# Kernel tuning notes

Measured on AMD Instinct MI355X. Metric: run time of the kernel, lower is better.

The kernel has to match this reference:

```python
import jax, jax.numpy as jnp
import numpy as np

K = 5          # reassembly kernel size
S = 2          # scale factor
ENC_PAD = 1    # encoder_kernel_size // 2


def _conv2d(x, w, pad):
    return jax.lax.conv_general_dilated(
        x, w, window_strides=(1, 1), padding=[(pad, pad), (pad, pad)],
        dimension_numbers=('NCHW', 'OIHW', 'NCHW'))


def setup_inputs() -> dict:
    key = jax.random.key(0)
    k1, k2, k3 = jax.random.split(key, 3)
    x = jax.random.normal(k1, (2, 256, 40, 40), dtype=jnp.float32)
    # channel compressor: xavier-uniform-ish 1x1 conv weight (64, 256, 1, 1)
    limit = np.sqrt(6.0 / (256 + 64)).astype(np.float32)
    w_comp = jax.random.uniform(k2, (64, 256, 1, 1), dtype=jnp.float32,
                                minval=-limit, maxval=limit)
    # content encoder: normal(0, 0.001), out = k^2*s^2 = 100 channels
    w_enc = 0.001 * jax.random.normal(k3, (100, 64, 3, 3), dtype=jnp.float32)
    return {"x": x, "w_comp": w_comp, "w_enc": w_enc}


def reference(x, w_comp, w_enc):
    b, c, h, w = x.shape
    k2 = K * K
    h_up, w_up = h * S, w * S

    # --- kernel prediction ---
    compressed = _conv2d(x, w_comp, 0)                # (b, 64, h, w)
    kern = _conv2d(compressed, w_enc, ENC_PAD)        # (b, k2*S^2, h, w)
    # pixel shuffle: (b, k2, S, S, h, w) -> (b, k2, h, S, w, S) -> (b, k2, h_up, w_up)
    kern = kern.reshape(b, k2, S, S, h, w).transpose(0, 1, 4, 2, 5, 3)
    kern = kern.reshape(b, k2, h_up * w_up)
    kern = jax.nn.softmax(kern, axis=1)               # softmax over k2

    # --- unfold (im2col, padding K//2) ---
    pad = K // 2
    xp = jnp.pad(x, ((0, 0), (0, 0), (pad, pad), (pad, pad)))
    # (b, c, k2, h, w): channel-major, kernel offsets inner (matches torch F.unfold)
    patches = jnp.stack([xp[:, :, i:i + h, j:j + w]
                         for i in range(K) for j in range(K)], axis=2)
    x_unfold = patches.reshape(b, c, k2, h * w)

    # --- reassembly (faithful to the torch 'efficient' path) ---
    # torch repeat_interleaves x_unfold S^2 times along the h*w axis and
    # multiplies with kernels flattened in (h_up*w_up) row-major order; that
    # pairing is exactly kern reshaped to (b, k2, h*w, S^2):
    kern4 = kern.reshape(b, k2, h * w, S * S)
    out = jnp.einsum('bckp,bkpd->bcpd', x_unfold, kern4)  # (b, c, h*w, S^2)
    return out.reshape(b, c, h_up, w_up)
```

## Files before the change

kernel.cpp:

```cpp
#include <hip/hip_runtime.h>

#define B   2
#define C   256
#define CM  64
#define CE  100
#define H   40
#define W   40
#define HW  1600
#define KK  25

__global__ __launch_bounds__(256) void k1_conv1x1(
    const float* __restrict__ x, const float* __restrict__ w,
    float* __restrict__ pc) {
  const int t = blockIdx.x, ich = blockIdx.y, b = blockIdx.z;
  __shared__ __align__(16) float xs[64 * 64];
  __shared__ __align__(16) float wsA[64 * 64];
  const int tid = threadIdx.x;

  const float4* x4 = (const float4*)(x + ((size_t)b * C + ich * 64) * HW + t * 64);
#pragma unroll
  for (int i = 0; i < 4; i++) {
    int idx = tid + i * 256;
    ((float4*)xs)[idx] = x4[(idx >> 4) * 400 + (idx & 15)];
  }
  const float4* w4 = (const float4*)w;
#pragma unroll
  for (int i = 0; i < 4; i++) {
    int idx = tid + i * 256;
    int icq = idx >> 6, oc = idx & 63;
    float4 f = w4[oc * 64 + ich * 16 + icq];
    wsA[(icq * 4 + 0) * 64 + oc] = f.x;
    wsA[(icq * 4 + 1) * 64 + oc] = f.y;
    wsA[(icq * 4 + 2) * 64 + oc] = f.z;
    wsA[(icq * 4 + 3) * 64 + oc] = f.w;
  }
  __syncthreads();

  const int ty = tid >> 4, tx = tid & 15;
  float acc[4][4];
#pragma unroll
  for (int i = 0; i < 4; i++)
#pragma unroll
    for (int j = 0; j < 4; j++) acc[i][j] = 0.f;

#pragma unroll 4
  for (int icl = 0; icl < 64; icl++) {
    float4 a = *(const float4*)&wsA[icl * 64 + ty * 4];
    float4 bb = *(const float4*)&xs[icl * 64 + tx * 4];
    float av[4] = {a.x, a.y, a.z, a.w};
    float bv[4] = {bb.x, bb.y, bb.z, bb.w};
#pragma unroll
    for (int i = 0; i < 4; i++)
#pragma unroll
      for (int j = 0; j < 4; j++) acc[i][j] += av[i] * bv[j];
  }

  float* o = pc + ((size_t)ich * B + b) * CM * HW + t * 64 + tx * 4;
#pragma unroll
  for (int j = 0; j < 4; j++)
    *(float4*)&o[(size_t)(ty * 4 + j) * HW] =
        make_float4(acc[j][0], acc[j][1], acc[j][2], acc[j][3]);
}

__global__ __launch_bounds__(256) void k2_conv3x3(
    const float* __restrict__ pc, const float* __restrict__ w,
    float* __restrict__ encP) {
  const int tile = blockIdx.x, ocq = blockIdx.y, icq = blockIdx.z;
  const int ty5 = tile / 5, tx5 = tile % 5;
  __shared__ __align__(16) float smem[3200 + 16 * 9 * 28];
  float* cs  = smem;
  float* wsb = smem + 3200;
  float* pacc = smem;
  const int tid = threadIdx.x;

  for (int i = tid; i < 3200; i += 256) {
    int bb = i / 1600, r = i - bb * 1600;
    int icl = r / 100, rr = r - icl * 100;
    int yy = rr / 10, xx = rr - yy * 10;
    int gy = ty5 * 8 + yy - 1, gx = tx5 * 8 + xx - 1;
    float v = 0.f;
    if (gy >= 0 && gy < H && gx >= 0 && gx < W) {
      int o = bb * 102400 + (icq * 16 + icl) * HW + gy * W + gx;
      v = pc[o] + pc[204800 + o] + pc[409600 + o] + pc[614400 + o];
    }
    cs[i] = v;
  }
  const float* wb = w + (size_t)(ocq * 25) * 576 + (size_t)(icq * 16) * 9;
  for (int i = tid; i < 3600; i += 256) {
    int ol = i / 144, r = i - ol * 144;
    wsb[r * 28 + ol] = wb[ol * 576 + r];
  }
  __syncthreads();

  const int wv = tid >> 6, lane = tid & 63, py = lane >> 3, px = lane & 7;
  float acc[50];
#pragma unroll
  for (int j = 0; j < 50; j++) acc[j] = 0.f;

#pragma unroll 1
  for (int t = 0; t < 4; t++) {
    const int icl = wv * 4 + t;
    const float* c0 = &cs[icl * 100 + py * 10 + px];
    const float* c1 = c0 + 1600;
    const float* wrow = &wsb[icl * 9 * 28];
#pragma unroll
    for (int dy = 0; dy < 3; dy++) {
#pragma unroll
      for (int dx = 0; dx < 3; dx++) {
        float x0 = c0[dy * 10 + dx];
        float x1 = c1[dy * 10 + dx];
        const float* wp = &wrow[(dy * 3 + dx) * 28];
        float4 w0 = *(const float4*)&wp[0],  w1 = *(const float4*)&wp[4];
        float4 w2 = *(const float4*)&wp[8],  w3 = *(const float4*)&wp[12];
        float4 w4v = *(const float4*)&wp[16], w5 = *(const float4*)&wp[20];
        float w6 = wp[24];
        acc[0]  += x0 * w0.x;  acc[1]  += x0 * w0.y;  acc[2]  += x0 * w0.z;  acc[3]  += x0 * w0.w;
        acc[4]  += x0 * w1.x;  acc[5]  += x0 * w1.y;  acc[6]  += x0 * w1.z;  acc[7]  += x0 * w1.w;
        acc[8]  += x0 * w2.x;  acc[9]  += x0 * w2.y;  acc[10] += x0 * w2.z;  acc[11] += x0 * w2.w;
        acc[12] += x0 * w3.x;  acc[13] += x0 * w3.y;  acc[14] += x0 * w3.z;  acc[15] += x0 * w3.w;
        acc[16] += x0 * w4v.x; acc[17] += x0 * w4v.y; acc[18] += x0 * w4v.z; acc[19] += x0 * w4v.w;
        acc[20] += x0 * w5.x;  acc[21] += x0 * w5.y;  acc[22] += x0 * w5.z;  acc[23] += x0 * w5.w;
        acc[24] += x0 * w6;
        acc[25] += x1 * w0.x;  acc[26] += x1 * w0.y;  acc[27] += x1 * w0.z;  acc[28] += x1 * w0.w;
        acc[29] += x1 * w1.x;  acc[30] += x1 * w1.y;  acc[31] += x1 * w1.z;  acc[32] += x1 * w1.w;
        acc[33] += x1 * w2.x;  acc[34] += x1 * w2.y;  acc[35] += x1 * w2.z;  acc[36] += x1 * w2.w;
        acc[37] += x1 * w3.x;  acc[38] += x1 * w3.y;  acc[39] += x1 * w3.z;  acc[40] += x1 * w3.w;
        acc[41] += x1 * w4v.x; acc[42] += x1 * w4v.y; acc[43] += x1 * w4v.z; acc[44] += x1 * w4v.w;
        acc[45] += x1 * w5.x;  acc[46] += x1 * w5.y;  acc[47] += x1 * w5.z;  acc[48] += x1 * w5.w;
        acc[49] += x1 * w6;
      }
    }
  }

  __syncthreads();
  if (wv == 1 || wv == 3) {
    const int slot = wv >> 1;
#pragma unroll
    for (int j = 0; j < 50; j++) pacc[slot * 3200 + j * 64 + lane] = acc[j];
  }
  __syncthreads();
  if (wv == 0 || wv == 2) {
    const int slot = wv >> 1;
#pragma unroll
    for (int j = 0; j < 50; j++) acc[j] += pacc[slot * 3200 + j * 64 + lane];
  }
  __syncthreads();
  if (wv == 2) {
#pragma unroll
    for (int j = 0; j < 50; j++) pacc[j * 64 + lane] = acc[j];
  }
  __syncthreads();
  if (wv == 0) {
    const int base_px = (ty5 * 8 + py) * W + tx5 * 8 + px;
#pragma unroll
    for (int bb = 0; bb < 2; bb++)
#pragma unroll
      for (int ol = 0; ol < 25; ol++)
        encP[(((size_t)icq * 2 + bb) * CE + ocq * 25 + ol) * HW + base_px] =
            acc[bb * 25 + ol] + pacc[(bb * 25 + ol) * 64 + lane];
  }
}

__global__ __launch_bounds__(256) void k3_reassemble(
    const float* __restrict__ x, const float* __restrict__ encP,
    float* __restrict__ out) {
  const int i0 = blockIdx.x >> 1;
  const int jh = blockIdx.x & 1;
  const int cq = blockIdx.y;
  const int b = blockIdx.z;

  __shared__ __align__(16) float wlds[20 * KK * 4];
  __shared__ float xsm[64 * 121];

  const int tid = threadIdx.x;

  if (tid < 80) {
    const int e = jh * 80 + tid;
    const int j0 = e >> 2, d = e & 3;
    const int off = ((e >= 80) ? 2 : 0) + (e & 1);
    const int col = ((e >= 80) ? (j0 - 20) : j0) * 2 + (d >> 1);
    const float* ep = encP + (size_t)b * CE * HW + i0 * W + col;
    float v[KK];
    float m = -1e30f;
#pragma unroll
    for (int k = 0; k < KK; k++) {
      int o = (k * 4 + off) * HW;
      v[k] = ep[o] + ep[320000 + o] + ep[640000 + o] + ep[960000 + o];
      m = fmaxf(m, v[k]);
    }
    float s = 0.f;
#pragma unroll
    for (int k = 0; k < KK; k++) {
      v[k] = expf(v[k] - m);
      s += v[k];
    }
    const float inv = 1.f / s;
    const int j0l = j0 - jh * 20;
#pragma unroll
    for (int k = 0; k < KK; k++) wlds[(j0l * KK + k) * 4 + d] = v[k] * inv;
  }

  const float* xb = x + ((size_t)b * C + cq * 64) * HW;
  for (int i = tid; i < 64 * 120; i += 256) {
    int c = i / 120;
    int rr = i % 120;
    int r = rr / 24, t = rr % 24;
    int gy = i0 - 2 + r;
    int gx = jh * 20 + t - 2;
    float v = 0.f;
    if (gy >= 0 && gy < H && gx >= 0 && gx < W) v = xb[c * HW + gy * W + gx];
    xsm[c * 121 + r * 24 + t] = v;
  }
  __syncthreads();

  const int wv = tid >> 6;
  const int lane = tid & 63;
  float* ob = out + (((size_t)b * C + cq * 64 + lane) * 6400) + i0 * 160;
  const float* xrow = &xsm[lane * 121];
#pragma unroll 1
  for (int jj = 0; jj < 5; jj++) {
    const int j0l = wv * 5 + jj;
    const int j0 = jh * 20 + j0l;
    float a0 = 0.f, a1 = 0.f, a2 = 0.f, a3 = 0.f;
#pragma unroll
    for (int ki = 0; ki < 5; ki++) {
#pragma unroll
      for (int kj = 0; kj < 5; kj++) {
        float xv = xrow[ki * 24 + j0l + kj];
        float4 w4 = *(const float4*)&wlds[(j0l * KK + ki * 5 + kj) * 4];
        a0 += xv * w4.x;
        a1 += xv * w4.y;
        a2 += xv * w4.z;
        a3 += xv * w4.w;
      }
    }
    float4 o = make_float4(a0, a1, a2, a3);
    *(float4*)&ob[j0 * 4] = o;
  }
}

extern "C" void kernel_launch(void* const* d_in, const int* in_sizes, int n_in,
                              void* d_out, int out_size, void* d_ws, size_t ws_size,
                              hipStream_t stream) {
  const float* x      = (const float*)d_in[0];
  const float* w_comp = (const float*)d_in[1];
  const float* w_enc  = (const float*)d_in[2];
  float* out = (float*)d_out;

  float* pc   = (float*)d_ws;
  float* encP = (float*)((char*)d_ws + 3276800);

  k1_conv1x1<<<dim3(25, 4, B), 256, 0, stream>>>(x, w_comp, pc);
  k2_conv3x3<<<dim3(25, 4, 4), 256, 0, stream>>>(pc, w_enc, encP);
  k3_reassemble<<<dim3(80, 4, B), 256, 0, stream>>>(x, encP, out);
}
```

Before: 109.7 us.

## Pre-transpose encoder weights, retile conv3x3 and reassembly across all channels

Adds a small kernel that transposes the 3x3 encoder weights into a padded layout in workspace, so the conv3x3 kernel reads weights straight from global memory with wave-uniform addresses instead of staging them in LDS. The conv3x3 grid doubles with smaller 8x4 spatial tiles and 25 accumulators per thread, which lowers register pressure and raises occupancy. The reassembly kernel is restructured so each block covers all 256 channels for 4 output columns. Each thread computes 4 channels times 4 sub-pixels, which reuses the softmax weights across more channels and cuts redundant softmax work. The cost is an extra kernel launch, and the reassembly's strided per-channel loads of x may coalesce poorly.

```diff
diff --git a/kernel.cpp b/kernel.cpp
--- a/kernel.cpp
+++ b/kernel.cpp
@@ -9,6 +9,16 @@
 #define HW  1600
 #define KK  25
 
+__global__ __launch_bounds__(256) void k0_wt(const float* __restrict__ w,
+                                             float* __restrict__ wT) {
+  int idx = blockIdx.x * 256 + threadIdx.x;
+  if (idx < 57600) {
+    int row = idx / 576, col = idx - row * 576;
+    int ocq = row / 25, ol = row - ocq * 25;
+    wT[((size_t)(ocq * 576 + col)) * 32 + ol] = w[idx];
+  }
+}
+
 __global__ __launch_bounds__(256) void k1_conv1x1(
     const float* __restrict__ x, const float* __restrict__ w,
     float* __restrict__ pc) {
@@ -63,21 +73,20 @@
 }
 
 __global__ __launch_bounds__(256) void k2_conv3x3(
-    const float* __restrict__ pc, const float* __restrict__ w,
+    const float* __restrict__ pc, const float* __restrict__ wT,
     float* __restrict__ encP) {
-  const int tile = blockIdx.x, ocq = blockIdx.y, icq = blockIdx.z;
-  const int ty5 = tile / 5, tx5 = tile % 5;
-  __shared__ __align__(16) float smem[3200 + 16 * 9 * 28];
-  float* cs  = smem;
-  float* wsb = smem + 3200;
+  const int t = blockIdx.x, ocq = blockIdx.y, icq = blockIdx.z;
+  const int ty = t / 10, tx = t - ty * 10;
+  __shared__ __align__(16) float smem[3200];
+  float* cs   = smem;
   float* pacc = smem;
   const int tid = threadIdx.x;
 
-  for (int i = tid; i < 3200; i += 256) {
-    int bb = i / 1600, r = i - bb * 1600;
-    int icl = r / 100, rr = r - icl * 100;
-    int yy = rr / 10, xx = rr - yy * 10;
-    int gy = ty5 * 8 + yy - 1, gx = tx5 * 8 + xx - 1;
+  for (int i = tid; i < 1920; i += 256) {
+    int bb = i / 960, r = i - bb * 960;
+    int icl = r / 60, rr = r - icl * 60;
+    int yy = rr / 6, xx = rr - yy * 6;
+    int gy = ty * 8 + yy - 1, gx = tx * 4 + xx - 1;
     float v = 0.f;
     if (gy >= 0 && gy < H && gx >= 0 && gx < W) {
       int o = bb * 102400 + (icq * 16 + icl) * HW + gy * W + gx;
@@ -85,100 +94,76 @@
     }
     cs[i] = v;
   }
-  const float* wb = w + (size_t)(ocq * 25) * 576 + (size_t)(icq * 16) * 9;
-  for (int i = tid; i < 3600; i += 256) {
-    int ol = i / 144, r = i - ol * 144;
-    wsb[r * 28 + ol] = wb[ol * 576 + r];
-  }
-  __syncthreads();
-
-  const int wv = tid >> 6, lane = tid & 63, py = lane >> 3, px = lane & 7;
-  float acc[50];
-#pragma unroll
-  for (int j = 0; j < 50; j++) acc[j] = 0.f;
-
-#pragma unroll 1
-  for (int t = 0; t < 4; t++) {
-    const int icl = wv * 4 + t;
-    const float* c0 = &cs[icl * 100 + py * 10 + px];
-    const float* c1 = c0 + 1600;
-    const float* wrow = &wsb[icl * 9 * 28];
-#pragma unroll
-    for (int dy = 0; dy < 3; dy++) {
+  __syncthreads();
+
+  const int wv = tid >> 6, lane = tid & 63;
+  const int bb = lane >> 5, py = (lane & 31) >> 2, px = lane & 3;
+  float acc[25];
+#pragma unroll
+  for (int j = 0; j < 25; j++) acc[j] = 0.f;
+
+  const float* wbase0 = wT + (size_t)((ocq * 4 + icq) * 16) * 288;
+
+#pragma unroll
+  for (int t4 = 0; t4 < 4; t4++) {
+    const int icl = __builtin_amdgcn_readfirstlane(wv * 4 + t4);
+    const float* c0 = &cs[(bb * 16 + icl) * 60 + py * 6 + px];
+    const float* wrow = wbase0 + icl * 288;
+#pragma unroll
+    for (int dy = 0; dy < 3; dy++)
 #pragma unroll
       for (int dx = 0; dx < 3; dx++) {
-        float x0 = c0[dy * 10 + dx];
-        float x1 = c1[dy * 10 + dx];
-        const float* wp = &wrow[(dy * 3 + dx) * 28];
-        float4 w0 = *(const float4*)&wp[0],  w1 = *(const float4*)&wp[4];
-        float4 w2 = *(const float4*)&wp[8],  w3 = *(const float4*)&wp[12];
-        float4 w4v = *(const float4*)&wp[16], w5 = *(const float4*)&wp[20];
-        float w6 = wp[24];
-        acc[0]  += x0 * w0.x;  acc[1]  += x0 * w0.y;  acc[2]  += x0 * w0.z;  acc[3]  += x0 * w0.w;
-        acc[4]  += x0 * w1.x;  acc[5]  += x0 * w1.y;  acc[6]  += x0 * w1.z;  acc[7]  += x0 * w1.w;
-        acc[8]  += x0 * w2.x;  acc[9]  += x0 * w2.y;  acc[10] += x0 * w2.z;  acc[11] += x0 * w2.w;
-        acc[12] += x0 * w3.x;  acc[13] += x0 * w3.y;  acc[14] += x0 * w3.z;  acc[15] += x0 * w3.w;
-        acc[16] += x0 * w4v.x; acc[17] += x0 * w4v.y; acc[18] += x0 * w4v.z; acc[19] += x0 * w4v.w;
-        acc[20] += x0 * w5.x;  acc[21] += x0 * w5.y;  acc[22] += x0 * w5.z;  acc[23] += x0 * w5.w;
-        acc[24] += x0 * w6;
-        acc[25] += x1 * w0.x;  acc[26] += x1 * w0.y;  acc[27] += x1 * w0.z;  acc[28] += x1 * w0.w;
-        acc[29] += x1 * w1.x;  acc[30] += x1 * w1.y;  acc[31] += x1 * w1.z;  acc[32] += x1 * w1.w;
-        acc[33] += x1 * w2.x;  acc[34] += x1 * w2.y;  acc[35] += x1 * w2.z;  acc[36] += x1 * w2.w;
-        acc[37] += x1 * w3.x;  acc[38] += x1 * w3.y;  acc[39] += x1 * w3.z;  acc[40] += x1 * w3.w;
-        acc[41] += x1 * w4v.x; acc[42] += x1 * w4v.y; acc[43] += x1 * w4v.z; acc[44] += x1 * w4v.w;
-        acc[45] += x1 * w5.x;  acc[46] += x1 * w5.y;  acc[47] += x1 * w5.z;  acc[48] += x1 * w5.w;
-        acc[49] += x1 * w6;
+        const float xv = c0[dy * 6 + dx];
+        const float* wq = wrow + (dy * 3 + dx) * 32;
+#pragma unroll
+        for (int j = 0; j < 25; j++) acc[j] = fmaf(xv, wq[j], acc[j]);
       }
-    }
   }
 
   __syncthreads();
   if (wv == 1 || wv == 3) {
     const int slot = wv >> 1;
 #pragma unroll
-    for (int j = 0; j < 50; j++) pacc[slot * 3200 + j * 64 + lane] = acc[j];
+    for (int j = 0; j < 25; j++) pacc[(slot * 25 + j) * 64 + lane] = acc[j];
   }
   __syncthreads();
   if (wv == 0 || wv == 2) {
     const int slot = wv >> 1;
 #pragma unroll
-    for (int j = 0; j < 50; j++) acc[j] += pacc[slot * 3200 + j * 64 + lane];
+    for (int j = 0; j < 25; j++) acc[j] += pacc[(slot * 25 + j) * 64 + lane];
   }
   __syncthreads();
   if (wv == 2) {
 #pragma unroll
-    for (int j = 0; j < 50; j++) pacc[j * 64 + lane] = acc[j];
+    for (int j = 0; j < 25; j++) pacc[j * 64 + lane] = acc[j];
   }
   __syncthreads();
   if (wv == 0) {
-    const int base_px = (ty5 * 8 + py) * W + tx5 * 8 + px;
-#pragma unroll
-    for (int bb = 0; bb < 2; bb++)
-#pragma unroll
-      for (int ol = 0; ol < 25; ol++)
-        encP[(((size_t)icq * 2 + bb) * CE + ocq * 25 + ol) * HW + base_px] =
-            acc[bb * 25 + ol] + pacc[(bb * 25 + ol) * 64 + lane];
+    const int base_px = (ty * 8 + py) * W + tx * 4 + px;
+#pragma unroll
+    for (int ol = 0; ol < 25; ol++)
+      encP[(((size_t)icq * 2 + bb) * CE + ocq * 25 + ol) * HW + base_px] =
+          acc[ol] + pacc[ol * 64 + lane];
   }
 }
 
 __global__ __launch_bounds__(256) void k3_reassemble(
     const float* __restrict__ x, const float* __restrict__ encP,
     float* __restrict__ out) {
-  const int i0 = blockIdx.x >> 1;
-  const int jh = blockIdx.x & 1;
-  const int cq = blockIdx.y;
-  const int b = blockIdx.z;
-
-  __shared__ __align__(16) float wlds[20 * KK * 4];
-  __shared__ float xsm[64 * 121];
-
+  const int i0 = blockIdx.x;
+  const int jq = blockIdx.y;
+  const int b  = blockIdx.z;
   const int tid = threadIdx.x;
 
-  if (tid < 80) {
-    const int e = jh * 80 + tid;
-    const int j0 = e >> 2, d = e & 3;
-    const int off = ((e >= 80) ? 2 : 0) + (e & 1);
-    const int col = ((e >= 80) ? (j0 - 20) : j0) * 2 + (d >> 1);
+  __shared__ __align__(16) float xsm[5 * 8 * 256];
+  __shared__ __align__(16) float wlds[4 * KK * 4];
+
+  if (tid < 16) {
+    const int j0l = tid >> 2, d = tid & 3;
+    const int j0 = jq * 4 + j0l;
+    const int t20 = (j0 >= 20) ? 1 : 0;
+    const int off = 2 * t20 + (d & 1);
+    const int col = (j0 - 20 * t20) * 2 + (d >> 1);
     const float* ep = encP + (size_t)b * CE * HW + i0 * W + col;
     float v[KK];
     float m = -1e30f;
@@ -195,48 +180,50 @@
       s += v[k];
     }
     const float inv = 1.f / s;
-    const int j0l = j0 - jh * 20;
 #pragma unroll
     for (int k = 0; k < KK; k++) wlds[(j0l * KK + k) * 4 + d] = v[k] * inv;
   }
 
-  const float* xb = x + ((size_t)b * C + cq * 64) * HW;
-  for (int i = tid; i < 64 * 120; i += 256) {
-    int c = i / 120;
-    int rr = i % 120;
-    int r = rr / 24, t = rr % 24;
-    int gy = i0 - 2 + r;
-    int gx = jh * 20 + t - 2;
-    float v = 0.f;
-    if (gy >= 0 && gy < H && gx >= 0 && gx < W) v = xb[c * HW + gy * W + gx];
-    xsm[c * 121 + r * 24 + t] = v;
-  }
-  __syncthreads();
-
-  const int wv = tid >> 6;
-  const int lane = tid & 63;
-  float* ob = out + (((size_t)b * C + cq * 64 + lane) * 6400) + i0 * 160;
-  const float* xrow = &xsm[lane * 121];
-#pragma unroll 1
-  for (int jj = 0; jj < 5; jj++) {
-    const int j0l = wv * 5 + jj;
-    const int j0 = jh * 20 + j0l;
-    float a0 = 0.f, a1 = 0.f, a2 = 0.f, a3 = 0.f;
+  {
+    const float* xb = x + ((size_t)b * C + tid) * HW;
+    const int gx0 = jq * 4 - 2;
 #pragma unroll
     for (int ki = 0; ki < 5; ki++) {
-#pragma unroll
-      for (int kj = 0; kj < 5; kj++) {
-        float xv = xrow[ki * 24 + j0l + kj];
-        float4 w4 = *(const float4*)&wlds[(j0l * KK + ki * 5 + kj) * 4];
-        a0 += xv * w4.x;
-        a1 += xv * w4.y;
-        a2 += xv * w4.z;
-        a3 += xv * w4.w;
+      const int gy = i0 - 2 + ki;
+      const bool rowok = (gy >= 0) && (gy < H);
+#pragma unroll
+      for (int cc = 0; cc < 8; cc++) {
+        const int gx = gx0 + cc;
+        float v = 0.f;
+        if (rowok && gx >= 0 && gx < W) v = xb[gy * W + gx];
+        xsm[(ki * 8 + cc) * 256 + tid] = v;
       }
     }
-    float4 o = make_float4(a0, a1, a2, a3);
-    *(float4*)&ob[j0 * 4] = o;
-  }
+  }
+  __syncthreads();
+
+  const int wv = tid >> 6, lane = tid & 63, ch0 = lane * 4;
+  float4 a0 = make_float4(0.f, 0.f, 0.f, 0.f);
+  float4 a1 = a0, a2 = a0, a3 = a0;
+
+#pragma unroll
+  for (int ki = 0; ki < 5; ki++)
+#pragma unroll
+    for (int kj = 0; kj < 5; kj++) {
+      float4 xv = *(const float4*)&xsm[(ki * 8 + wv + kj) * 256 + ch0];
+      float4 w4 = *(const float4*)&wlds[(wv * KK + ki * 5 + kj) * 4];
+      a0.x += xv.x * w4.x; a0.y += xv.y * w4.x; a0.z += xv.z * w4.x; a0.w += xv.w * w4.x;
+      a1.x += xv.x * w4.y; a1.y += xv.y * w4.y; a1.z += xv.z * w4.y; a1.w += xv.w * w4.y;
+      a2.x += xv.x * w4.z; a2.y += xv.y * w4.z; a2.z += xv.z * w4.z; a2.w += xv.w * w4.z;
+      a3.x += xv.x * w4.w; a3.y += xv.y * w4.w; a3.z += xv.z * w4.w; a3.w += xv.w * w4.w;
+    }
+
+  const int j0 = jq * 4 + wv;
+  float* ob = out + ((size_t)b * C + ch0) * 6400 + i0 * 160 + j0 * 4;
+  *(float4*)&ob[0]     = make_float4(a0.x, a1.x, a2.x, a3.x);
+  *(float4*)&ob[6400]  = make_float4(a0.y, a1.y, a2.y, a3.y);
+  *(float4*)&ob[12800] = make_float4(a0.z, a1.z, a2.z, a3.z);
+  *(float4*)&ob[19200] = make_float4(a0.w, a1.w, a2.w, a3.w);
 }
 
 extern "C" void kernel_launch(void* const* d_in, const int* in_sizes, int n_in,
@@ -249,8 +236,10 @@
 
   float* pc   = (float*)d_ws;
   float* encP = (float*)((char*)d_ws + 3276800);
-
+  float* wT   = (float*)((char*)d_ws + 8396800);
+
+  k0_wt<<<dim3(225), 256, 0, stream>>>(w_enc, wT);
   k1_conv1x1<<<dim3(25, 4, B), 256, 0, stream>>>(x, w_comp, pc);
-  k2_conv3x3<<<dim3(25, 4, 4), 256, 0, stream>>>(pc, w_enc, encP);
-  k3_reassemble<<<dim3(80, 4, B), 256, 0, stream>>>(x, encP, out);
-}
+  k2_conv3x3<<<dim3(50, 4, 4), 256, 0, stream>>>(pc, wT, encP);
+  k3_reassemble<<<dim3(40, 10, B), 256, 0, stream>>>(x, encP, out);
+}
```

New measurement: 130.3 us. 1.19x slower.
